# Kernel tuning notes

Measured on AMD Instinct MI355X. Metric: run time of the kernel, lower is better.

Reference implementation:

```python
import jax, jax.numpy as jnp
import numpy as np

L = 4096
EMBED = 512
KEY = 512
VAL = 512
HEADS = 8

def _linear_params(key, fan_in, fan_out):
    k1, k2 = jax.random.split(key)
    w = jax.random.normal(k1, (fan_in, fan_out), jnp.float32) * 0.02
    b = jax.random.normal(k2, (fan_out,), jnp.float32) * 0.02
    return w, b

def setup_inputs() -> dict:
    key = jax.random.key(0)
    ks = jax.random.split(key, 9)
    x = jax.random.normal(ks[0], (L, EMBED), jnp.float32)
    shortest_path = jax.random.normal(ks[1], (L, L), jnp.float32)
    wq_w, wq_b = _linear_params(ks[2], EMBED, KEY)
    wk_w, wk_b = _linear_params(ks[3], EMBED, KEY)
    wv_w, wv_b = _linear_params(ks[4], EMBED, VAL)
    qp_w, qp_b = _linear_params(ks[5], KEY, KEY)
    kp_w, kp_b = _linear_params(ks[6], KEY, KEY)
    vp_w, vp_b = _linear_params(ks[7], VAL, VAL)
    out_w, out_b = _linear_params(ks[8], VAL, EMBED)
    return dict(x=x, shortest_path=shortest_path,
                wq_w=wq_w, wq_b=wq_b, wk_w=wk_w, wk_b=wk_b, wv_w=wv_w, wv_b=wv_b,
                qp_w=qp_w, qp_b=qp_b, kp_w=kp_w, kp_b=kp_b, vp_w=vp_w, vp_b=vp_b,
                out_w=out_w, out_b=out_b)

def reference(x, shortest_path, wq_w, wq_b, wk_w, wk_b, wv_w, wv_b,
              qp_w, qp_b, kp_w, kp_b, vp_w, vp_b, out_w, out_b):
    H = HEADS
    dh = KEY // H   # q/k head dim
    dv = VAL // H   # v head dim
    # two-stage projections
    q = (x @ wq_w + wq_b) @ qp_w + qp_b          # [L, KEY]
    k = (x @ wk_w + wk_b) @ kp_w + kp_b          # [L, KEY]
    v = (x @ wv_w + wv_b) @ vp_w + vp_b          # [L, VAL]
    q = q.reshape(L, H, dh).transpose(1, 0, 2)   # [H, L, dh]
    k = k.reshape(L, H, dh).transpose(1, 0, 2)
    v = v.reshape(L, H, dv).transpose(1, 0, 2)   # [H, L, dv]
    att = jnp.einsum('hqd,hkd->hqk', q, k) / jnp.sqrt(jnp.float32(dh))  # [H, L, L]
    sp = jax.nn.softmax(shortest_path, axis=-1) * 0.5                   # [L, L]
    att = jax.nn.softmax(att + sp[None, :, :], axis=-1)                 # [H, L, L]
    out = jnp.einsum('hqk,hkd->hqd', att, v)     # [H, L, dv]
    out = out.transpose(1, 0, 2).reshape(L, VAL)
    return out @ out_w + out_b                   # [L, EMBED]
```

## Files before the change

kernel.cpp:

```cpp
#include <hip/hip_runtime.h>
#include <hip/hip_fp16.h>

typedef _Float16 f16;
typedef __fp16 fp16x2 __attribute__((ext_vector_type(2)));
typedef _Float16 f16x4 __attribute__((ext_vector_type(4)));
typedef _Float16 f16x8 __attribute__((ext_vector_type(8)));
typedef float f32x4 __attribute__((ext_vector_type(4)));
typedef float f32x16 __attribute__((ext_vector_type(16)));

#define L_SEQ 4096
#define D_MODEL 512
#define KVSPLIT 4
#define C_SCALE 0.18033688f

template <typename T, typename F>
__device__ __forceinline__ T bitcast(F x) { return __builtin_bit_cast(T, x); }

__device__ __forceinline__ void gload16(const void* g, void* l) {
  __builtin_amdgcn_global_load_lds((const __attribute__((address_space(1))) void*)g,
                                   (__attribute__((address_space(3))) void*)l, 16, 0, 0);
}

__global__ void cvt4_kernel(const float* __restrict__ s0, const float* __restrict__ s1,
                            const float* __restrict__ s2, const float* __restrict__ s3,
                            f16* __restrict__ d0, f16* __restrict__ d1,
                            f16* __restrict__ d2, f16* __restrict__ d3) {
  const float* s; f16* d; int n4; float sc = 1.0f;
  switch (blockIdx.z) {
    case 0: s = s0; d = d0; n4 = 524288; break;
    case 1: s = s1; d = d1; n4 = 65536; sc = C_SCALE; break;
    case 2: s = s2; d = d2; n4 = 65536; break;
    default: s = s3; d = d3; n4 = 65536; break;
  }
  for (int i = blockIdx.x * 256 + threadIdx.x; i < n4; i += 131072) {
    float4 v = ((const float4*)s)[i];
    f16x4 o;
    o[0] = (f16)(v.x * sc); o[1] = (f16)(v.y * sc);
    o[2] = (f16)(v.z * sc); o[3] = (f16)(v.w * sc);
    ((f16x4*)d)[i] = o;
  }
}

__global__ void transpose4_kernel(
    const float* __restrict__ s0, const float* __restrict__ s1,
    const float* __restrict__ s2, const float* __restrict__ s3,
    f16* __restrict__ d0, f16* __restrict__ d1, f16* __restrict__ d2, f16* __restrict__ d3)
{
  const float* s; f16* d;
  switch (blockIdx.z) {
    case 0: s = s0; d = d0; break;
    case 1: s = s1; d = d1; break;
    case 2: s = s2; d = d2; break;
    default: s = s3; d = d3; break;
  }
  __shared__ float tl[32][33];
  const int bx = blockIdx.x * 32, by = blockIdx.y * 32;
  const int tx = threadIdx.x, ty = threadIdx.y;
  #pragma unroll
  for (int i = 0; i < 4; ++i)
    tl[ty + i * 8][tx] = s[(size_t)(by + ty + i * 8) * 512 + bx + tx];
  __syncthreads();
  #pragma unroll
  for (int i = 0; i < 4; ++i)
    d[(size_t)(bx + ty + i * 8) * 512 + by + tx] = (f16)tl[tx][ty + i * 8];
}

template<int MODE, int BM>
__device__ __forceinline__ void gemm_core(
    const f16* __restrict__ A, const f16* __restrict__ BT,
    const float* __restrict__ bias, void* __restrict__ Cv,
    int M, int N, int K, f16* As, f16* Bs)
{
  constexpr int MI = BM / 32;
  const int t = threadIdx.x;
  const int w = t >> 6;
  const int bm = blockIdx.x * BM, bn = blockIdx.y * 64;
  const int m0 = (w >> 1) * (BM / 2), n0 = (w & 1) * 32;
  const int lane = t & 63, lr = lane & 15, lg = lane >> 4;

  f32x4 zf = {0.f, 0.f, 0.f, 0.f};
  f32x4 acc[MI][2];
  #pragma unroll
  for (int i = 0; i < MI; ++i)
    #pragma unroll
    for (int j = 0; j < 2; ++j)
      acc[i][j] = zf;

  const int arow = t >> 2, achk = t & 3;
  const f16* gA = A + (size_t)(bm + arow) * K + achk * 8;
  const f16* gB = BT + (size_t)(bn + arow) * K + achk * 8;
  f16* lA = As + w * 512;
  f16* lB = Bs + w * 512;

  for (int k0 = 0; k0 < K; k0 += 32) {
    gload16(gA + k0, lA);
    if constexpr (BM == 128) gload16(gA + (size_t)64 * K + k0, lA + 2048);
    gload16(gB + k0, lB);
    __syncthreads();
    f16x8 af[MI], bfv[2];
    #pragma unroll
    for (int i = 0; i < MI; ++i)
      af[i] = *(const f16x8*)&As[(m0 + i * 16 + lr) * 32 + lg * 8];
    #pragma unroll
    for (int j = 0; j < 2; ++j)
      bfv[j] = *(const f16x8*)&Bs[(n0 + j * 16 + lr) * 32 + lg * 8];
    #pragma unroll
    for (int i = 0; i < MI; ++i)
      #pragma unroll
      for (int j = 0; j < 2; ++j)
        acc[i][j] = __builtin_amdgcn_mfma_f32_16x16x32_f16(af[i], bfv[j], acc[i][j], 0, 0, 0);
    __syncthreads();
  }

  #pragma unroll
  for (int j = 0; j < 2; ++j) {
    const int gn = bn + n0 + j * 16 + lr;
    const float bv = (MODE == 3) ? 0.f : bias[gn];
    #pragma unroll
    for (int i = 0; i < MI; ++i) {
      const int gmb = bm + m0 + i * 16 + lg * 4;
      if constexpr (MODE == 0 || MODE == 3) {
        f16* C = (f16*)Cv;
        #pragma unroll
        for (int r = 0; r < 4; ++r)
          C[(size_t)(gmb + r) * N + gn] = (f16)(acc[i][j][r] + bv);
      } else if constexpr (MODE == 1) {
        f16* C = (f16*)Cv;
        f16x4 u;
        u[0] = (f16)(acc[i][j][0] + bv);
        u[1] = (f16)(acc[i][j][1] + bv);
        u[2] = (f16)(acc[i][j][2] + bv);
        u[3] = (f16)(acc[i][j][3] + bv);
        *(f16x4*)&C[(size_t)gn * M + gmb] = u;
      } else {
        float* C = (float*)Cv;
        #pragma unroll
        for (int r = 0; r < 4; ++r)
          C[(size_t)(gmb + r) * N + gn] = acc[i][j][r] + bv;
      }
    }
  }
}

template<int MODE, int BM>
__global__ __launch_bounds__(256) void gemm_bt_kernel(
    const f16* __restrict__ A, const f16* __restrict__ BT,
    const float* __restrict__ bias, void* __restrict__ Cv, int M, int N, int K)
{
  __shared__ __attribute__((aligned(16))) f16 As[BM * 32];
  __shared__ __attribute__((aligned(16))) f16 Bs[64 * 32];
  gemm_core<MODE, BM>(A, BT, bias, Cv, M, N, K, As, Bs);
}

__global__ __launch_bounds__(256) void wcombine_kernel(
    const f16* __restrict__ qpT, const f16* __restrict__ kpT, const f16* __restrict__ vpT,
    const f16* __restrict__ wq16, const f16* __restrict__ wk16, const f16* __restrict__ wv16,
    f16* __restrict__ WqT, f16* __restrict__ WkT, f16* __restrict__ WvT)
{
  __shared__ __attribute__((aligned(16))) f16 As[128 * 32];
  __shared__ __attribute__((aligned(16))) f16 Bs[64 * 32];
  const f16* A; const f16* B; f16* C;
  switch (blockIdx.z) {
    case 0: A = qpT; B = wq16; C = WqT; break;
    case 1: A = kpT; B = wk16; C = WkT; break;
    default: A = vpT; B = wv16; C = WvT; break;
  }
  gemm_core<3, 128>(A, B, nullptr, C, 512, 512, 512, As, Bs);
}

__global__ void bcombine_kernel(
    const float* __restrict__ wq_b, const float* __restrict__ wk_b, const float* __restrict__ wv_b,
    const f16* __restrict__ qpT, const f16* __restrict__ kpT, const f16* __restrict__ vpT,
    const float* __restrict__ qp_b, const float* __restrict__ kp_b, const float* __restrict__ vp_b,
    float* __restrict__ bc)
{
  const float* b1; const f16* WT; const float* b2;
  switch (blockIdx.z) {
    case 0: b1 = wq_b; WT = qpT; b2 = qp_b; break;
    case 1: b1 = wk_b; WT = kpT; b2 = kp_b; break;
    default: b1 = wv_b; WT = vpT; b2 = vp_b; break;
  }
  const int o = blockIdx.x * 256 + threadIdx.x;
  const f16* row = WT + (size_t)o * 512;
  float s = 0.f;
  #pragma unroll 8
  for (int m = 0; m < 512; ++m)
    s += b1[m] * (float)row[m];
  const float sc = (blockIdx.z == 0) ? C_SCALE : 1.0f;
  bc[blockIdx.z * 512 + o] = (s + b2[o]) * sc;
}

__global__ __launch_bounds__(256) void gemm_qkv_kernel(
    const f16* __restrict__ x,
    const f16* __restrict__ WqT, const f16* __restrict__ WkT, const f16* __restrict__ WvT,
    const float* __restrict__ bc,
    f16* __restrict__ q_f, f16* __restrict__ k_f, f16* __restrict__ vT)
{
  __shared__ __attribute__((aligned(16))) f16 As[128 * 32];
  __shared__ __attribute__((aligned(16))) f16 Bs[64 * 32];
  const int z = blockIdx.z;
  if (z == 2)
    gemm_core<1, 128>(x, WvT, bc + 1024, vT, 4096, 512, 512, As, Bs);
  else if (z == 1)
    gemm_core<0, 128>(x, WkT, bc + 512, k_f, 4096, 512, 512, As, Bs);
  else
    gemm_core<0, 128>(x, WqT, bc, q_f, 4096, 512, 512, As, Bs);
}

__global__ __launch_bounds__(512) void sp_bias_kernel(
    const float* __restrict__ spg, f16* __restrict__ bt)
{
  __shared__ __attribute__((aligned(16))) f16 ex[16 * 4104];
  __shared__ float sums[16];
  const int t = threadIdx.x;

  {
    const int row = t >> 5, j = t & 31;
    const float4* srow = (const float4*)(spg + (size_t)(blockIdx.x * 16 + row) * L_SEQ);
    f16* dst = ex + row * 4104;
    float ssum = 0.f;
    #pragma unroll 4
    for (int c = 0; c < 32; ++c) {
      float4 v = srow[c * 32 + j];
      float e0 = __expf(v.x), e1 = __expf(v.y), e2 = __expf(v.z), e3 = __expf(v.w);
      ssum += (e0 + e1) + (e2 + e3);
      f16x4 u;
      u[0] = (f16)e0; u[1] = (f16)e1; u[2] = (f16)e2; u[3] = (f16)e3;
      *(f16x4*)&dst[(c * 32 + j) * 4] = u;
    }
    ssum += __shfl_xor(ssum, 1, 64);
    ssum += __shfl_xor(ssum, 2, 64);
    ssum += __shfl_xor(ssum, 4, 64);
    ssum += __shfl_xor(ssum, 8, 64);
    ssum += __shfl_xor(ssum, 16, 64);
    if (j == 0) sums[row] = ssum;
  }
  __syncthreads();

  const int hi = t & 1, qloc = (t >> 1) & 15, s16 = (t >> 5) & 1;
  const float sc = 0.5f / sums[qloc];
  const int qt5 = blockIdx.x >> 1;
  const int q31 = ((blockIdx.x & 1) << 4) + qloc;
  const f16* exr = ex + qloc * 4104 + s16 * 16 + hi * 8;
  f16* ob = bt + (size_t)qt5 * 131072 + s16 * 512 + q31 * 16 + hi * 8;
  #pragma unroll 4
  for (int i = 0; i < 16; ++i) {
    const int kt5 = (t >> 6) + i * 8;
    f16x8 v = *(const f16x8*)&exr[kt5 * 32];
    f16x8 u;
    #pragma unroll
    for (int e = 0; e < 8; ++e)
      u[e] = (f16)__log2f(fmaf((float)v[e], sc, 1.0f));
    *(f16x8*)&ob[(size_t)kt5 * 1024] = u;
  }
}

__global__ __launch_bounds__(256, 4) void attn3_kernel(
    const f16* __restrict__ qg, const f16* __restrict__ kg,
    const f16* __restrict__ vTg, const f16* __restrict__ bt,
    f16* __restrict__ opart, float* __restrict__ rspart)
{
  __shared__ __attribute__((aligned(16))) f16 Ks[2 * 4096];
  __shared__ __attribute__((aligned(16))) f16 Vs[2 * 4096];

  const int t = threadIdx.x;
  const int w = t >> 6, lane = t & 63;
  const int l31 = lane & 31, hi = lane >> 5;
  const int b = blockIdx.x;
  const int h = (b >> 3) & 7;
  const int g = (b & 7) + ((b >> 6) << 3);
  const int qt = g & 31;
  const int z = g >> 5;
  const int q0w = qt * 128 + w * 32;
  const int kvbase = z * (L_SEQ / KVSPLIT);
  const int NST = (L_SEQ / KVSPLIT) / 64;

  f16x8 qf[4];
  #pragma unroll
  for (int dk = 0; dk < 4; ++dk)
    qf[dk] = *(const f16x8*)&qg[(size_t)(q0w + l31) * D_MODEL + h * 64 + dk * 16 + hi * 8];

  const int srow0 = t >> 3, srow1 = 32 + (t >> 3), q16 = t & 7;
  const f16* ksrc0 = kg + h * 64 + (size_t)(kvbase + srow0) * D_MODEL + ((q16 ^ (srow0 & 7)) * 8);
  const f16* ksrc1 = kg + h * 64 + (size_t)(kvbase + srow1) * D_MODEL + ((q16 ^ (srow1 & 7)) * 8);
  const f16* vsrc0 = vTg + (size_t)(h * 64 + srow0) * L_SEQ + kvbase + (q16 ^ (srow0 & 7)) * 8;
  const f16* vsrc1 = vTg + (size_t)(h * 64 + srow1) * L_SEQ + kvbase + (q16 ^ (srow1 & 7)) * 8;

  #define STAGE(buf, stp)                                                      \
    do {                                                                       \
      const size_t ko = (size_t)(stp) * 64 * D_MODEL, vo = (size_t)(stp) * 64; \
      gload16(ksrc0 + ko, &Ks[(buf) * 4096 + w * 512]);                        \
      gload16(ksrc1 + ko, &Ks[(buf) * 4096 + 2048 + w * 512]);                 \
      gload16(vsrc0 + vo, &Vs[(buf) * 4096 + w * 512]);                        \
      gload16(vsrc1 + vo, &Vs[(buf) * 4096 + 2048 + w * 512]);                 \
    } while (0)

  const int sw23 = (l31 & ~12) | ((l31 & 4) << 1) | ((l31 & 8) >> 1);
  const int r7 = sw23 & 7;
  const int krow0 = sw23 * 64, krow1 = krow0 + 2048;
  const int vr7 = l31 & 7;
  const int vrow0 = l31 * 64, vrow1 = vrow0 + 2048;

  const f16* bb = bt + (size_t)(q0w >> 5) * 131072 + l31 * 16 + hi * 8;
  const int kvb5 = kvbase >> 5;

  f32x16 zz = {0,0,0,0,0,0,0,0,0,0,0,0,0,0,0,0};
  f32x16 o0 = zz, o1 = zz;
  float rs0 = 0.f, rs1 = 0.f;
  const fp16x2 one2 = {(__fp16)1.0f, (__fp16)1.0f};

  STAGE(0, 0);
  __syncthreads();

  for (int st = 0; st < NST; ++st) {
    const int buf = st & 1;

    const f16* bs = bb + (size_t)(kvb5 + st * 2) * 1024;
    f16x8 bl[4];
    bl[0] = *(const f16x8*)(bs);
    bl[1] = *(const f16x8*)(bs + 512);
    bl[2] = *(const f16x8*)(bs + 1024);
    bl[3] = *(const f16x8*)(bs + 1536);
    __builtin_amdgcn_sched_barrier(0);

    if (st + 1 < NST) STAGE(buf ^ 1, st + 1);

    f32x16 s0 = zz, s1 = zz;
    const f16* kb = &Ks[buf * 4096];
    #pragma unroll
    for (int dk = 0; dk < 4; ++dk) {
      const int ch = ((dk * 2 + hi) ^ r7) * 8;
      f16x8 k0 = *(const f16x8*)&kb[krow0 + ch];
      f16x8 k1 = *(const f16x8*)&kb[krow1 + ch];
      s0 = __builtin_amdgcn_mfma_f32_32x32x16_f16(k0, qf[dk], s0, 0, 0, 0);
      s1 = __builtin_amdgcn_mfma_f32_32x32x16_f16(k1, qf[dk], s1, 0, 0, 0);
    }

    f16x8 pa[4];
    #pragma unroll
    for (int q = 0; q < 4; ++q) {
      const f32x16& s = (q >> 1) ? s1 : s0;
      const int sh = q & 1;
      union { f16x8 v; fp16x2 h2[4]; } ub; ub.v = bl[q];
      union { fp16x2 h2[4]; f16x8 v; } up;
      #pragma unroll
      for (int e2 = 0; e2 < 4; ++e2) {
        fp16x2 s2 = __builtin_amdgcn_cvt_pkrtz(s[sh * 8 + e2 * 2], s[sh * 8 + e2 * 2 + 1]);
        __half2 p2 = h2exp2(__hadd2(bitcast<__half2>(s2), bitcast<__half2>(ub.h2[e2])));
        fp16x2 pp = bitcast<fp16x2>(p2);
        up.h2[e2] = pp;
        if (e2 & 1) rs1 = __builtin_amdgcn_fdot2(pp, one2, rs1, false);
        else        rs0 = __builtin_amdgcn_fdot2(pp, one2, rs0, false);
      }
      pa[q] = up.v;
    }

    const f16* vb = &Vs[buf * 4096];
    #pragma unroll
    for (int kk = 0; kk < 4; ++kk) {
      const int ch = ((kk * 2 + hi) ^ vr7) * 8;
      f16x8 v0 = *(const f16x8*)&vb[vrow0 + ch];
      f16x8 v1 = *(const f16x8*)&vb[vrow1 + ch];
      o0 = __builtin_amdgcn_mfma_f32_32x32x16_f16(pa[kk], v0, o0, 0, 0, 0);
      o1 = __builtin_amdgcn_mfma_f32_32x32x16_f16(pa[kk], v1, o1, 0, 0, 0);
    }
    __syncthreads();
  }
  #undef STAGE

  float rs = rs0 + rs1;
  rs += __shfl_xor(rs, 32, 64);
  f16* op = opart + (size_t)z * (L_SEQ * D_MODEL);
  #pragma unroll
  for (int dg = 0; dg < 2; ++dg) {
    const f32x16& o = dg ? o1 : o0;
    #pragma unroll
    for (int r = 0; r < 16; ++r) {
      const int q = q0w + (r & 3) + 8 * (r >> 2) + 4 * hi;
      op[(size_t)q * D_MODEL + h * 64 + dg * 32 + l31] = (f16)o[r];
    }
  }
  if (hi == 0)
    rspart[((size_t)z * 8 + h) * L_SEQ + q0w + l31] = rs;
}

__global__ void combine4_kernel(const f16* __restrict__ opart,
                                const float* __restrict__ rspart,
                                f16* __restrict__ attout)
{
  const int idx = blockIdx.x * 256 + threadIdx.x;
  const int q = idx >> 6;
  const int d = (idx & 63) << 3;
  const int h = d >> 6;
  float rsum = 0.f;
  #pragma unroll
  for (int zz = 0; zz < KVSPLIT; ++zz)
    rsum += rspart[((size_t)zz * 8 + h) * L_SEQ + q];
  const float inv = 1.f / rsum;
  float acc[8] = {0,0,0,0,0,0,0,0};
  #pragma unroll
  for (int zz = 0; zz < KVSPLIT; ++zz) {
    f16x8 v = *(const f16x8*)&opart[(size_t)zz * (L_SEQ * D_MODEL) + (size_t)q * D_MODEL + d];
    #pragma unroll
    for (int e = 0; e < 8; ++e) acc[e] += (float)v[e];
  }
  f16x8 u;
  #pragma unroll
  for (int e = 0; e < 8; ++e) u[e] = (f16)(acc[e] * inv);
  *(f16x8*)&attout[(size_t)q * D_MODEL + d] = u;
}

extern "C" void kernel_launch(void* const* d_in, const int* in_sizes, int n_in,
                              void* d_out, int out_size, void* d_ws, size_t ws_size,
                              hipStream_t stream)
{
  (void)in_sizes; (void)n_in; (void)out_size; (void)ws_size;

  const float* x    = (const float*)d_in[0];
  const float* sp   = (const float*)d_in[1];
  const float* wq_w = (const float*)d_in[2];
  const float* wq_b = (const float*)d_in[3];
  const float* wk_w = (const float*)d_in[4];
  const float* wk_b = (const float*)d_in[5];
  const float* wv_w = (const float*)d_in[6];
  const float* wv_b = (const float*)d_in[7];
  const float* qp_w = (const float*)d_in[8];
  const float* qp_b = (const float*)d_in[9];
  const float* kp_w = (const float*)d_in[10];
  const float* kp_b = (const float*)d_in[11];
  const float* vp_w = (const float*)d_in[12];
  const float* vp_b = (const float*)d_in[13];
  const float* out_w = (const float*)d_in[14];
  const float* out_b = (const float*)d_in[15];

  const size_t MB = 1048576;
  char* ws = (char*)d_ws;
  f16*   x_f    = (f16*)(ws + 0);
  f16*   qpT    = (f16*)(ws + 4 * MB);
  f16*   kpT    = (f16*)(ws + 4 * MB + 524288);
  f16*   vpT    = (f16*)(ws + 5 * MB);
  f16*   wq16   = (f16*)(ws + 6 * MB);
  f16*   wk16   = (f16*)(ws + 6 * MB + 524288);
  f16*   wv16   = (f16*)(ws + 7 * MB);
  f16*   WqT    = (f16*)(ws + 7 * MB + 524288);
  f16*   WkT    = (f16*)(ws + 8 * MB);
  f16*   WvT    = (f16*)(ws + 8 * MB + 524288);
  float* bc     = (float*)(ws + 9 * MB);
  f16*   opart  = (f16*)(ws + 0);
  f16*   q_f    = (f16*)(ws + 16 * MB);
  f16*   attout = (f16*)(ws + 16 * MB);
  f16*   k_f    = (f16*)(ws + 20 * MB);
  f16*   vT     = (f16*)(ws + 24 * MB);
  float* rspart = (float*)(ws + 28 * MB);
  f16*   bt     = (f16*)(ws + 28 * MB + 524288);
  f16*   outT   = (f16*)(ws + 60 * MB + 524288);

  cvt4_kernel<<<dim3(512, 1, 4), 256, 0, stream>>>(x, wq_w, wk_w, wv_w,
                                                   x_f, wq16, wk16, wv16);
  transpose4_kernel<<<dim3(16, 16, 4), dim3(32, 8), 0, stream>>>(
      qp_w, kp_w, vp_w, out_w, qpT, kpT, vpT, outT);
  sp_bias_kernel<<<256, 512, 0, stream>>>(sp, bt);

  wcombine_kernel<<<dim3(4, 8, 3), 256, 0, stream>>>(qpT, kpT, vpT,
                                                     wq16, wk16, wv16,
                                                     WqT, WkT, WvT);
  bcombine_kernel<<<dim3(2, 1, 3), 256, 0, stream>>>(wq_b, wk_b, wv_b,
                                                     qpT, kpT, vpT,
                                                     qp_b, kp_b, vp_b, bc);
  gemm_qkv_kernel<<<dim3(32, 8, 3), 256, 0, stream>>>(x_f, WqT, WkT, WvT, bc,
                                                      q_f, k_f, vT);

  attn3_kernel<<<dim3(1024), 256, 0, stream>>>(q_f, k_f, vT, bt,
                                               opart, rspart);
  combine4_kernel<<<1024, 256, 0, stream>>>(opart, rspart, attout);

  gemm_bt_kernel<2, 64><<<dim3(64, 8), 256, 0, stream>>>(attout, outT, out_b,
                                                         d_out, 4096, 512, 512);
}
```

Baseline: 135.7 us.

## Merge prep and weight-combine launches, add MFMA wave priority in attention

```diff
diff --git a/kernel.cpp b/kernel.cpp
--- a/kernel.cpp
+++ b/kernel.cpp
@@ -21,48 +21,56 @@
                                    (__attribute__((address_space(3))) void*)l, 16, 0, 0);
 }
 
-__global__ void cvt4_kernel(const float* __restrict__ s0, const float* __restrict__ s1,
-                            const float* __restrict__ s2, const float* __restrict__ s3,
-                            f16* __restrict__ d0, f16* __restrict__ d1,
-                            f16* __restrict__ d2, f16* __restrict__ d3) {
-  const float* s; f16* d; int n4; float sc = 1.0f;
-  switch (blockIdx.z) {
-    case 0: s = s0; d = d0; n4 = 524288; break;
-    case 1: s = s1; d = d1; n4 = 65536; sc = C_SCALE; break;
-    case 2: s = s2; d = d2; n4 = 65536; break;
-    default: s = s3; d = d3; n4 = 65536; break;
-  }
-  for (int i = blockIdx.x * 256 + threadIdx.x; i < n4; i += 131072) {
-    float4 v = ((const float4*)s)[i];
-    f16x4 o;
-    o[0] = (f16)(v.x * sc); o[1] = (f16)(v.y * sc);
-    o[2] = (f16)(v.z * sc); o[3] = (f16)(v.w * sc);
-    ((f16x4*)d)[i] = o;
-  }
-}
-
-__global__ void transpose4_kernel(
-    const float* __restrict__ s0, const float* __restrict__ s1,
-    const float* __restrict__ s2, const float* __restrict__ s3,
-    f16* __restrict__ d0, f16* __restrict__ d1, f16* __restrict__ d2, f16* __restrict__ d3)
-{
-  const float* s; f16* d;
-  switch (blockIdx.z) {
-    case 0: s = s0; d = d0; break;
-    case 1: s = s1; d = d1; break;
-    case 2: s = s2; d = d2; break;
-    default: s = s3; d = d3; break;
-  }
-  __shared__ float tl[32][33];
-  const int bx = blockIdx.x * 32, by = blockIdx.y * 32;
-  const int tx = threadIdx.x, ty = threadIdx.y;
-  #pragma unroll
-  for (int i = 0; i < 4; ++i)
-    tl[ty + i * 8][tx] = s[(size_t)(by + ty + i * 8) * 512 + bx + tx];
-  __syncthreads();
-  #pragma unroll
-  for (int i = 0; i < 4; ++i)
-    d[(size_t)(bx + ty + i * 8) * 512 + by + tx] = (f16)tl[tx][ty + i * 8];
+__global__ __launch_bounds__(256) void prep_kernel(
+    const float* __restrict__ x, const float* __restrict__ wq_w,
+    const float* __restrict__ wk_w, const float* __restrict__ wv_w,
+    const float* __restrict__ qp_w, const float* __restrict__ kp_w,
+    const float* __restrict__ vp_w, const float* __restrict__ out_w,
+    f16* __restrict__ x_f, f16* __restrict__ wq16,
+    f16* __restrict__ wk16, f16* __restrict__ wv16,
+    f16* __restrict__ qpT, f16* __restrict__ kpT,
+    f16* __restrict__ vpT, f16* __restrict__ outT)
+{
+  const int bid = blockIdx.x, t = threadIdx.x;
+  if (bid < 704) {
+    const float* s; f16* d; int i, n4, stride; float sc = 1.0f;
+    if (bid < 512) {
+      s = x; d = x_f; i = bid * 256 + t; n4 = 524288; stride = 131072;
+    } else {
+      const int widx = (bid - 512) >> 6;
+      s = (widx == 0) ? wq_w : (widx == 1) ? wk_w : wv_w;
+      d = (widx == 0) ? wq16 : (widx == 1) ? wk16 : wv16;
+      if (widx == 0) sc = C_SCALE;
+      i = ((bid - 512) & 63) * 256 + t; n4 = 65536; stride = 16384;
+    }
+    for (; i < n4; i += stride) {
+      float4 v = ((const float4*)s)[i];
+      f16x4 o;
+      o[0] = (f16)(v.x * sc); o[1] = (f16)(v.y * sc);
+      o[2] = (f16)(v.z * sc); o[3] = (f16)(v.w * sc);
+      ((f16x4*)d)[i] = o;
+    }
+  } else {
+    __shared__ float tl[32][33];
+    const int tt = bid - 704;
+    const int mat = tt >> 8, tile = tt & 255;
+    const float* s; f16* d;
+    switch (mat) {
+      case 0: s = qp_w; d = qpT; break;
+      case 1: s = kp_w; d = kpT; break;
+      case 2: s = vp_w; d = vpT; break;
+      default: s = out_w; d = outT; break;
+    }
+    const int bx = (tile & 15) * 32, by = (tile >> 4) * 32;
+    const int tx = t & 31, ty = t >> 5;
+    #pragma unroll
+    for (int i = 0; i < 4; ++i)
+      tl[ty + i * 8][tx] = s[(size_t)(by + ty + i * 8) * 512 + bx + tx];
+    __syncthreads();
+    #pragma unroll
+    for (int i = 0; i < 4; ++i)
+      d[(size_t)(bx + ty + i * 8) * 512 + by + tx] = (f16)tl[tx][ty + i * 8];
+  }
 }
 
 template<int MODE, int BM>
@@ -152,42 +160,43 @@
   gemm_core<MODE, BM>(A, BT, bias, Cv, M, N, K, As, Bs);
 }
 
-__global__ __launch_bounds__(256) void wcombine_kernel(
+__global__ __launch_bounds__(256) void wbcombine_kernel(
     const f16* __restrict__ qpT, const f16* __restrict__ kpT, const f16* __restrict__ vpT,
     const f16* __restrict__ wq16, const f16* __restrict__ wk16, const f16* __restrict__ wv16,
-    f16* __restrict__ WqT, f16* __restrict__ WkT, f16* __restrict__ WvT)
+    f16* __restrict__ WqT, f16* __restrict__ WkT, f16* __restrict__ WvT,
+    const float* __restrict__ wq_b, const float* __restrict__ wk_b, const float* __restrict__ wv_b,
+    const float* __restrict__ qp_b, const float* __restrict__ kp_b, const float* __restrict__ vp_b,
+    float* __restrict__ bc)
 {
   __shared__ __attribute__((aligned(16))) f16 As[128 * 32];
   __shared__ __attribute__((aligned(16))) f16 Bs[64 * 32];
-  const f16* A; const f16* B; f16* C;
-  switch (blockIdx.z) {
-    case 0: A = qpT; B = wq16; C = WqT; break;
-    case 1: A = kpT; B = wk16; C = WkT; break;
-    default: A = vpT; B = wv16; C = WvT; break;
-  }
-  gemm_core<3, 128>(A, B, nullptr, C, 512, 512, 512, As, Bs);
-}
-
-__global__ void bcombine_kernel(
-    const float* __restrict__ wq_b, const float* __restrict__ wk_b, const float* __restrict__ wv_b,
-    const f16* __restrict__ qpT, const f16* __restrict__ kpT, const f16* __restrict__ vpT,
-    const float* __restrict__ qp_b, const float* __restrict__ kp_b, const float* __restrict__ vp_b,
-    float* __restrict__ bc)
-{
-  const float* b1; const f16* WT; const float* b2;
-  switch (blockIdx.z) {
-    case 0: b1 = wq_b; WT = qpT; b2 = qp_b; break;
-    case 1: b1 = wk_b; WT = kpT; b2 = kp_b; break;
-    default: b1 = wv_b; WT = vpT; b2 = vp_b; break;
-  }
-  const int o = blockIdx.x * 256 + threadIdx.x;
-  const f16* row = WT + (size_t)o * 512;
-  float s = 0.f;
-  #pragma unroll 8
-  for (int m = 0; m < 512; ++m)
-    s += b1[m] * (float)row[m];
-  const float sc = (blockIdx.z == 0) ? C_SCALE : 1.0f;
-  bc[blockIdx.z * 512 + o] = (s + b2[o]) * sc;
+  const int z = blockIdx.z;
+  if (z < 3) {
+    const f16* A; const f16* B; f16* C;
+    switch (z) {
+      case 0: A = qpT; B = wq16; C = WqT; break;
+      case 1: A = kpT; B = wk16; C = WkT; break;
+      default: A = vpT; B = wv16; C = WvT; break;
+    }
+    gemm_core<3, 128>(A, B, nullptr, C, 512, 512, 512, As, Bs);
+  } else {
+    if (blockIdx.x >= 2 || blockIdx.y != 0) return;
+    const int zz = z - 3;
+    const float* b1; const f16* WT; const float* b2;
+    switch (zz) {
+      case 0: b1 = wq_b; WT = qpT; b2 = qp_b; break;
+      case 1: b1 = wk_b; WT = kpT; b2 = kp_b; break;
+      default: b1 = wv_b; WT = vpT; b2 = vp_b; break;
+    }
+    const int o = blockIdx.x * 256 + threadIdx.x;
+    const f16* row = WT + (size_t)o * 512;
+    float s = 0.f;
+    #pragma unroll 8
+    for (int m = 0; m < 512; ++m)
+      s += b1[m] * (float)row[m];
+    const float sc = (zz == 0) ? C_SCALE : 1.0f;
+    bc[zz * 512 + o] = (s + b2[o]) * sc;
+  }
 }
 
 __global__ __launch_bounds__(256) void gemm_qkv_kernel(
@@ -325,16 +334,25 @@
 
     if (st + 1 < NST) STAGE(buf ^ 1, st + 1);
 
-    f32x16 s0 = zz, s1 = zz;
+    f32x16 s0, s1;
     const f16* kb = &Ks[buf * 4096];
-    #pragma unroll
-    for (int dk = 0; dk < 4; ++dk) {
+    __builtin_amdgcn_s_setprio(1);
+    {
+      const int ch0 = (hi ^ r7) * 8;
+      f16x8 k0 = *(const f16x8*)&kb[krow0 + ch0];
+      f16x8 k1 = *(const f16x8*)&kb[krow1 + ch0];
+      s0 = __builtin_amdgcn_mfma_f32_32x32x16_f16(k0, qf[0], zz, 0, 0, 0);
+      s1 = __builtin_amdgcn_mfma_f32_32x32x16_f16(k1, qf[0], zz, 0, 0, 0);
+    }
+    #pragma unroll
+    for (int dk = 1; dk < 4; ++dk) {
       const int ch = ((dk * 2 + hi) ^ r7) * 8;
       f16x8 k0 = *(const f16x8*)&kb[krow0 + ch];
       f16x8 k1 = *(const f16x8*)&kb[krow1 + ch];
       s0 = __builtin_amdgcn_mfma_f32_32x32x16_f16(k0, qf[dk], s0, 0, 0, 0);
       s1 = __builtin_amdgcn_mfma_f32_32x32x16_f16(k1, qf[dk], s1, 0, 0, 0);
     }
+    __builtin_amdgcn_s_setprio(0);
 
     f16x8 pa[4];
     #pragma unroll
@@ -356,6 +374,7 @@
     }
 
     const f16* vb = &Vs[buf * 4096];
+    __builtin_amdgcn_s_setprio(1);
     #pragma unroll
     for (int kk = 0; kk < 4; ++kk) {
       const int ch = ((kk * 2 + hi) ^ vr7) * 8;
@@ -364,6 +383,7 @@
       o0 = __builtin_amdgcn_mfma_f32_32x32x16_f16(pa[kk], v0, o0, 0, 0, 0);
       o1 = __builtin_amdgcn_mfma_f32_32x32x16_f16(pa[kk], v1, o1, 0, 0, 0);
     }
+    __builtin_amdgcn_s_setprio(0);
     __syncthreads();
   }
   #undef STAGE
@@ -455,18 +475,16 @@
   f16*   bt     = (f16*)(ws + 28 * MB + 524288);
   f16*   outT   = (f16*)(ws + 60 * MB + 524288);
 
-  cvt4_kernel<<<dim3(512, 1, 4), 256, 0, stream>>>(x, wq_w, wk_w, wv_w,
-                                                   x_f, wq16, wk16, wv16);
-  transpose4_kernel<<<dim3(16, 16, 4), dim3(32, 8), 0, stream>>>(
-      qp_w, kp_w, vp_w, out_w, qpT, kpT, vpT, outT);
+  prep_kernel<<<1728, 256, 0, stream>>>(x, wq_w, wk_w, wv_w,
+                                        qp_w, kp_w, vp_w, out_w,
+                                        x_f, wq16, wk16, wv16,
+                                        qpT, kpT, vpT, outT);
   sp_bias_kernel<<<256, 512, 0, stream>>>(sp, bt);
 
-  wcombine_kernel<<<dim3(4, 8, 3), 256, 0, stream>>>(qpT, kpT, vpT,
-                                                     wq16, wk16, wv16,
-                                                     WqT, WkT, WvT);
-  bcombine_kernel<<<dim3(2, 1, 3), 256, 0, stream>>>(wq_b, wk_b, wv_b,
-                                                     qpT, kpT, vpT,
-                                                     qp_b, kp_b, vp_b, bc);
+  wbcombine_kernel<<<dim3(4, 8, 6), 256, 0, stream>>>(
+      qpT, kpT, vpT, wq16, wk16, wv16, WqT, WkT, WvT,
+      wq_b, wk_b, wv_b, qp_b, kp_b, vp_b, bc);
+
   gemm_qkv_kernel<<<dim3(32, 8, 3), 256, 0, stream>>>(x_f, WqT, WkT, WvT, bc,
                                                       q_f, k_f, vT);
 
```

Result: faster. 126.0 us (-7.1%).
